# Kernel tuning notes

Hardware: AMD Instinct MI355X
Metric: run time of the kernel (lower is better)

Reference implementation:

```python
import math
import jax, jax.numpy as jnp
import numpy as np

N = 50000      # num nodes
E = 400000     # num edges
IN = 128       # in_channels
HID = 64       # hidden_channels
HEADS = 4
OUT = 32       # out_channels
TDIM = 16      # time_dim
NEG_SLOPE = 0.2
EPS = 1e-5


def setup_inputs() -> dict:
    key = jax.random.key(0)
    ks = jax.random.split(key, 20)
    s = 0.05
    # Fourier time encoder: Linear(1, TDIM) with freq-pattern weight
    freq = np.exp(np.arange(0, TDIM, 2, dtype=np.float32) * -(math.log(10000.0) / TDIM))
    tw = np.zeros((TDIM,), dtype=np.float32)
    tw[0::2] = freq
    tw[1::2] = freq
    return {
        "x": jax.random.normal(ks[0], (N, IN), jnp.float32),
        "edge_index": jax.random.randint(ks[1], (2, E), 0, N, jnp.int64),
        "edge_time": jax.random.uniform(ks[2], (E,), jnp.float32),
        "time_w": jnp.asarray(tw),
        "time_b": jax.random.normal(ks[3], (TDIM,), jnp.float32) * s,
        "proj_w": jax.random.normal(ks[4], (IN + TDIM, IN), jnp.float32) * s,
        "proj_b": jax.random.normal(ks[5], (IN,), jnp.float32) * s,
        "W1": jax.random.normal(ks[6], (IN, HEADS * HID), jnp.float32) * s,
        "a_src1": jax.random.normal(ks[7], (HEADS, HID), jnp.float32) * s,
        "a_dst1": jax.random.normal(ks[8], (HEADS, HID), jnp.float32) * s,
        "b1": jax.random.normal(ks[9], (HEADS * HID,), jnp.float32) * s,
        "g1": jnp.ones((HEADS * HID,), jnp.float32),
        "be1": jnp.zeros((HEADS * HID,), jnp.float32),
        "W2": jax.random.normal(ks[10], (HEADS * HID, OUT), jnp.float32) * s,
        "a_src2": jax.random.normal(ks[11], (1, OUT), jnp.float32) * s,
        "a_dst2": jax.random.normal(ks[12], (1, OUT), jnp.float32) * s,
        "b2": jax.random.normal(ks[13], (OUT,), jnp.float32) * s,
        "g2": jnp.ones((OUT,), jnp.float32),
        "be2": jnp.zeros((OUT,), jnp.float32),
    }


def layer_norm(h, g, b):
    mu = jnp.mean(h, axis=-1, keepdims=True)
    var = jnp.mean(jnp.square(h - mu), axis=-1, keepdims=True)
    return (h - mu) * jax.lax.rsqrt(var + EPS) * g + b


def gat_conv(x, src, dst, W, a_src, a_dst, bias, heads, ch, concat):
    """PyG GATConv (self-loops pre-appended in src/dst), inference (no dropout)."""
    n = x.shape[0]
    h = (x @ W).reshape(n, heads, ch)                       # [N,H,C]
    al_s = jnp.sum(h * a_src, axis=-1)                      # [N,H]
    al_d = jnp.sum(h * a_dst, axis=-1)                      # [N,H]
    e = al_s[src] + al_d[dst]                               # [Etot,H]
    e = jnp.where(e > 0, e, NEG_SLOPE * e)                  # leaky_relu
    m = jax.ops.segment_max(e, dst, num_segments=n)         # scatter-softmax
    ex = jnp.exp(e - m[dst])
    denom = jax.ops.segment_sum(ex, dst, num_segments=n)
    alpha = ex / denom[dst]                                 # [Etot,H]
    out = jax.ops.segment_sum(h[src] * alpha[:, :, None], dst, num_segments=n)  # [N,H,C]
    out = out.reshape(n, heads * ch) if concat else jnp.mean(out, axis=1)
    return out + bias


def reference(x, edge_index, edge_time, time_w, time_b, proj_w, proj_b,
              W1, a_src1, a_dst1, b1, g1, be1,
              W2, a_src2, a_dst2, b2, g2, be2):
    src, dst = edge_index[0], edge_index[1]
    # Fourier time encoding of edge timestamps
    tp = edge_time[:, None] * time_w + time_b               # [E,TDIM]
    even = (jnp.arange(TDIM) % 2) == 0
    t_enc = jnp.where(even, jnp.sin(tp), jnp.cos(tp))       # [E,TDIM]
    # scatter_reduce_(mean, include_self=True) onto source nodes: sum/(count+1)
    t_sum = jax.ops.segment_sum(t_enc, src, num_segments=N)
    cnt = jax.ops.segment_sum(jnp.ones((E,), x.dtype), src, num_segments=N)
    node_time = t_sum / (cnt + 1.0)[:, None]
    xin = jnp.concatenate([x, node_time], axis=-1) @ proj_w + proj_b  # [N,IN]
    # add self loops (PyG GATConv default)
    loop = jnp.arange(N, dtype=src.dtype)
    src2 = jnp.concatenate([src, loop])
    dst2 = jnp.concatenate([dst, loop])
    h = gat_conv(xin, src2, dst2, W1, a_src1, a_dst1, b1, HEADS, HID, True)
    h = jax.nn.elu(h)
    h = layer_norm(h, g1, be1)
    h = gat_conv(h, src2, dst2, W2, a_src2, a_dst2, b2, 1, OUT, False)
    h = layer_norm(h, g2, be2)
    return h
```

## Files before the change

kernel.cpp:

```cpp
#include <hip/hip_runtime.h>
#include <math.h>

#define NN 50000
#define EE 400000
#define INC 128
#define TD 16
#define H1C 256
#define OUTC 32
#define NEG 0.2f
#define PAD 64

#define EB 391
#define WB 160
#define PB 782

typedef _Float16 f16;
typedef __attribute__((ext_vector_type(8))) _Float16 f16x8;
typedef __attribute__((ext_vector_type(2))) _Float16 f16x2;
typedef __attribute__((ext_vector_type(4))) float f32x4;

__device__ __forceinline__ float leaky(float x) { return x > 0.f ? x : NEG * x; }
__device__ __forceinline__ float sel4f(const float4& v, int h) {
  return h == 0 ? v.x : h == 1 ? v.y : h == 2 ? v.z : v.w;
}

__global__ __launch_bounds__(256) void k_rank_proj(
    const int* __restrict__ ei, const float* __restrict__ et,
    int* __restrict__ deg_dst, int* __restrict__ deg_src,
    int* __restrict__ src_pad, float* __restrict__ et_pad,
    const float* __restrict__ W1, const float* __restrict__ W2,
    f16* __restrict__ W1T, f16* __restrict__ W2T,
    const float* __restrict__ x, const float* __restrict__ pw,
    const float* __restrict__ pb, f16* __restrict__ xin) {
  __shared__ f16 A[64 * 136];
  int tid = threadIdx.x;
  int b = blockIdx.x;
  if (b < EB) {
    int gid = b * 256 + tid;
    if (gid < EE / 4) {
      int4 sv = *(const int4*)(ei + gid * 4);
      int4 dv = *(const int4*)(ei + EE + gid * 4);
      float4 tv = *(const float4*)(et + gid * 4);
      int rd0 = atomicAdd(&deg_dst[dv.x], 1);
      int rd1 = atomicAdd(&deg_dst[dv.y], 1);
      int rd2 = atomicAdd(&deg_dst[dv.z], 1);
      int rd3 = atomicAdd(&deg_dst[dv.w], 1);
      int rs0 = atomicAdd(&deg_src[sv.x], 1);
      int rs1 = atomicAdd(&deg_src[sv.y], 1);
      int rs2 = atomicAdd(&deg_src[sv.z], 1);
      int rs3 = atomicAdd(&deg_src[sv.w], 1);
      if (rd0 < PAD) src_pad[dv.x * PAD + rd0] = sv.x;
      if (rd1 < PAD) src_pad[dv.y * PAD + rd1] = sv.y;
      if (rd2 < PAD) src_pad[dv.z * PAD + rd2] = sv.z;
      if (rd3 < PAD) src_pad[dv.w * PAD + rd3] = sv.w;
      if (rs0 < PAD) et_pad[sv.x * PAD + rs0] = tv.x;
      if (rs1 < PAD) et_pad[sv.y * PAD + rs1] = tv.y;
      if (rs2 < PAD) et_pad[sv.z * PAD + rs2] = tv.z;
      if (rs3 < PAD) et_pad[sv.w * PAD + rs3] = tv.w;
    }
    return;
  }
  if (b < EB + WB) {
    int idx = (b - EB) * 256 + tid;
    if (idx < 32768) {
      int c = idx >> 7, k = idx & 127;
      W1T[idx] = (f16)W1[k * 256 + c];
    } else {
      int i3 = idx - 32768;
      int c = i3 >> 8, k = i3 & 255;
      W2T[i3] = (f16)W2[k * 32 + c];
    }
    return;
  }
  int n0 = (b - EB - WB) * 64;
  int l = tid & 63, w = tid >> 6;
  for (int ci = tid; ci < 1024; ci += 256) {
    int r = ci >> 4, c8 = (ci & 15) * 8;
    int n = n0 + r;
    f16x8 hv = {};
    if (n < NN) {
      float4 v0 = *(const float4*)(x + (size_t)n * INC + c8);
      float4 v1 = *(const float4*)(x + (size_t)n * INC + c8 + 4);
      hv[0] = (f16)v0.x; hv[1] = (f16)v0.y; hv[2] = (f16)v0.z; hv[3] = (f16)v0.w;
      hv[4] = (f16)v1.x; hv[5] = (f16)v1.y; hv[6] = (f16)v1.z; hv[7] = (f16)v1.w;
    }
    *(f16x8*)(A + r * 136 + c8) = hv;
  }
  int r16 = l & 15, g = l >> 4;
  f16x8 breg[2][4];
  #pragma unroll
  for (int jj = 0; jj < 2; ++jj) {
    int col = w * 32 + jj * 16 + r16;
    #pragma unroll
    for (int kk = 0; kk < 4; ++kk)
      #pragma unroll
      for (int t = 0; t < 8; ++t)
        breg[jj][kk][t] = (f16)pw[(size_t)(kk * 32 + g * 8 + t) * 128 + col];
  }
  f32x4 acc[4][2];
  #pragma unroll
  for (int i = 0; i < 4; ++i)
    #pragma unroll
    for (int jj = 0; jj < 2; ++jj) acc[i][jj] = (f32x4){0.f, 0.f, 0.f, 0.f};
  __syncthreads();
  #pragma unroll
  for (int kk = 0; kk < 4; ++kk)
    #pragma unroll
    for (int i = 0; i < 4; ++i) {
      f16x8 a = *(const f16x8*)(A + (i * 16 + r16) * 136 + kk * 32 + g * 8);
      acc[i][0] = __builtin_amdgcn_mfma_f32_16x16x32_f16(a, breg[0][kk], acc[i][0], 0, 0, 0);
      acc[i][1] = __builtin_amdgcn_mfma_f32_16x16x32_f16(a, breg[1][kk], acc[i][1], 0, 0, 0);
    }
  #pragma unroll
  for (int i = 0; i < 4; ++i)
    #pragma unroll
    for (int jj = 0; jj < 2; ++jj) {
      int col = w * 32 + jj * 16 + r16;
      float bj = pb[col];
      #pragma unroll
      for (int q = 0; q < 4; ++q) {
        int row = n0 + i * 16 + g * 4 + q;
        if (row < NN) xin[(size_t)row * INC + col] = (f16)(acc[i][jj][q] + bj);
      }
    }
}

__global__ __launch_bounds__(256) void k_time_add(
    const int* __restrict__ deg_src, const float* __restrict__ et_pad,
    const float* __restrict__ tw, const float* __restrict__ tb,
    const float* __restrict__ pw, f16* __restrict__ xin) {
  __shared__ float nt[4][16];
  __shared__ float pwl[2048];
  int tid = threadIdx.x;
  for (int i = tid; i < 2048; i += 256) pwl[i] = pw[16384 + i];
  int lane = tid & 63, wid = tid >> 6;
  int n = blockIdx.x * 4 + wid;
  int cnt = min(deg_src[n], PAD);
  int k = lane & 15, g = lane >> 4;
  float w = tw[k], b = tb[k];
  bool isc = (k & 1);
  float v = 0.f;
  const float* ep = et_pad + (size_t)n * PAD;
  for (int i = g; i < cnt; i += 4) {
    float tp = ep[i] * w + b;
    v += isc ? __cosf(tp) : __sinf(tp);
  }
  v += __shfl_xor(v, 16);
  v += __shfl_xor(v, 32);
  if (lane < 16) nt[wid][k] = v / (float)(cnt + 1);
  __syncthreads();
  int c0 = lane * 2;
  float d0 = 0.f, d1 = 0.f;
  #pragma unroll
  for (int t = 0; t < 16; ++t) {
    float ntv = nt[wid][t];
    d0 = fmaf(ntv, pwl[t * 128 + c0], d0);
    d1 = fmaf(ntv, pwl[t * 128 + c0 + 1], d1);
  }
  f16x2* xp = (f16x2*)(xin + (size_t)n * INC + c0);
  f16x2 old = *xp;
  f16x2 nw;
  nw[0] = (f16)((float)old[0] + d0);
  nw[1] = (f16)((float)old[1] + d1);
  *xp = nw;
}

__global__ __launch_bounds__(256) void k_h1g(const f16* __restrict__ xin,
                                             const f16* __restrict__ W1T,
                                             const float* __restrict__ as1,
                                             const float* __restrict__ ad1,
                                             f16* __restrict__ h1,
                                             float* __restrict__ als,
                                             float* __restrict__ ald) {
  __shared__ f16 A[64 * 136];
  int tid = threadIdx.x, l = tid & 63, w = tid >> 6;
  int n0 = blockIdx.x * 64;
  f16x8 zero = {};
  for (int ci = tid; ci < 1024; ci += 256) {
    int r = ci >> 4, c8 = (ci & 15) * 8;
    int n = n0 + r;
    f16x8 v = (n < NN) ? *(const f16x8*)(xin + (size_t)n * INC + c8) : zero;
    *(f16x8*)(A + r * 136 + c8) = v;
  }
  int r16 = l & 15, g = l >> 4;
  f16x8 breg[4][4];
  #pragma unroll
  for (int jj = 0; jj < 4; ++jj) {
    int col = w * 64 + jj * 16 + r16;
    #pragma unroll
    for (int kk = 0; kk < 4; ++kk)
      breg[jj][kk] = *(const f16x8*)(W1T + col * 128 + kk * 32 + g * 8);
  }
  f32x4 acc[4][4];
  #pragma unroll
  for (int i = 0; i < 4; ++i)
    #pragma unroll
    for (int jj = 0; jj < 4; ++jj) acc[i][jj] = (f32x4){0.f, 0.f, 0.f, 0.f};
  __syncthreads();
  #pragma unroll
  for (int kk = 0; kk < 4; ++kk)
    #pragma unroll
    for (int i = 0; i < 4; ++i) {
      f16x8 a = *(const f16x8*)(A + (i * 16 + r16) * 136 + kk * 32 + g * 8);
      #pragma unroll
      for (int jj = 0; jj < 4; ++jj)
        acc[i][jj] = __builtin_amdgcn_mfma_f32_16x16x32_f16(a, breg[jj][kk], acc[i][jj], 0, 0, 0);
    }
  #pragma unroll
  for (int i = 0; i < 4; ++i)
    #pragma unroll
    for (int jj = 0; jj < 4; ++jj) {
      int col = w * 64 + jj * 16 + r16;
      #pragma unroll
      for (int q = 0; q < 4; ++q) {
        int row = n0 + i * 16 + g * 4 + q;
        if (row < NN) h1[(size_t)row * H1C + col] = (f16)acc[i][jj][q];
      }
    }
  float asc[4], adc[4];
  #pragma unroll
  for (int jj = 0; jj < 4; ++jj) {
    int col = w * 64 + jj * 16 + r16;
    asc[jj] = as1[col];
    adc[jj] = ad1[col];
  }
  #pragma unroll
  for (int i = 0; i < 4; ++i)
    #pragma unroll
    for (int q = 0; q < 4; ++q) {
      float ps = 0.f, pd = 0.f;
      #pragma unroll
      for (int jj = 0; jj < 4; ++jj) {
        ps = fmaf(acc[i][jj][q], asc[jj], ps);
        pd = fmaf(acc[i][jj][q], adc[jj], pd);
      }
      #pragma unroll
      for (int o = 1; o < 16; o <<= 1) {
        ps += __shfl_xor(ps, o);
        pd += __shfl_xor(pd, o);
      }
      int row = n0 + i * 16 + g * 4 + q;
      if (r16 == 0 && row < NN) {
        als[row * 4 + w] = ps;
        ald[row * 4 + w] = pd;
      }
    }
}

__global__ __launch_bounds__(256) void k_h2g(const f16* __restrict__ ln1,
                                             const f16* __restrict__ W2T,
                                             const float* __restrict__ as2,
                                             const float* __restrict__ ad2,
                                             f16* __restrict__ h2,
                                             float* __restrict__ als2,
                                             float* __restrict__ ald2) {
  __shared__ f16 A[64 * 264];
  int tid = threadIdx.x, l = tid & 63, w = tid >> 6;
  int n0 = blockIdx.x * 64;
  f16x8 zero = {};
  for (int ci = tid; ci < 2048; ci += 256) {
    int r = ci >> 5, c8 = (ci & 31) * 8;
    int n = n0 + r;
    f16x8 v = (n < NN) ? *(const f16x8*)(ln1 + (size_t)n * H1C + c8) : zero;
    *(f16x8*)(A + r * 264 + c8) = v;
  }
  int r16 = l & 15, g = l >> 4;
  f16x8 breg[2][8];
  #pragma unroll
  for (int jj = 0; jj < 2; ++jj) {
    int col = jj * 16 + r16;
    #pragma unroll
    for (int kk = 0; kk < 8; ++kk)
      breg[jj][kk] = *(const f16x8*)(W2T + col * 256 + kk * 32 + g * 8);
  }
  f32x4 acc[2];
  acc[0] = (f32x4){0.f, 0.f, 0.f, 0.f};
  acc[1] = (f32x4){0.f, 0.f, 0.f, 0.f};
  __syncthreads();
  #pragma unroll
  for (int kk = 0; kk < 8; ++kk) {
    f16x8 a = *(const f16x8*)(A + (w * 16 + r16) * 264 + kk * 32 + g * 8);
    acc[0] = __builtin_amdgcn_mfma_f32_16x16x32_f16(a, breg[0][kk], acc[0], 0, 0, 0);
    acc[1] = __builtin_amdgcn_mfma_f32_16x16x32_f16(a, breg[1][kk], acc[1], 0, 0, 0);
  }
  #pragma unroll
  for (int jj = 0; jj < 2; ++jj)
    #pragma unroll
    for (int q = 0; q < 4; ++q) {
      int row = n0 + w * 16 + g * 4 + q;
      int col = jj * 16 + r16;
      if (row < NN) h2[(size_t)row * OUTC + col] = (f16)acc[jj][q];
    }
  float as_0 = as2[r16], as_1 = as2[16 + r16];
  float ad_0 = ad2[r16], ad_1 = ad2[16 + r16];
  #pragma unroll
  for (int q = 0; q < 4; ++q) {
    float ps = acc[0][q] * as_0 + acc[1][q] * as_1;
    float pd = acc[0][q] * ad_0 + acc[1][q] * ad_1;
    #pragma unroll
    for (int o = 1; o < 16; o <<= 1) {
      ps += __shfl_xor(ps, o);
      pd += __shfl_xor(pd, o);
    }
    int row = n0 + w * 16 + g * 4 + q;
    if (r16 == 0 && row < NN) {
      als2[row] = ps;
      ald2[row] = pd;
    }
  }
}

__global__ __launch_bounds__(256) void k_agg1(
    const int* __restrict__ deg_dst, const int* __restrict__ src_pad,
    const f16* __restrict__ h1, const float* __restrict__ als,
    const float* __restrict__ ald, const float* __restrict__ b1,
    const float* __restrict__ g1, const float* __restrict__ be1,
    f16* __restrict__ ln1) {
  __shared__ int s_s[8][32];
  __shared__ float s_e[8][128];
  int tid = threadIdx.x;
  int grp = tid >> 5, l32 = tid & 31;
  int n = blockIdx.x * 8 + grp;
  int cnt = min(deg_dst[n], PAD);
  const int* sp = src_pad + (size_t)n * PAD;
  const float4 adv = *(const float4*)(ald + n * 4);
  int hh = l32 >> 3;
  int c0 = l32 * 8;
  float adh = sel4f(adv, hh);
  float seh = __expf(leaky(als[n * 4 + hh] + adh));

  f16x2 accA[4] = {}, accB[4] = {}, accC[4] = {}, accD[4] = {};
  float d = 0.f;
  for (int base = 0; base < cnt; base += 32) {
    int p = base + l32;
    if (p < cnt) {
      int sv = sp[p];
      const float4 a = *(const float4*)(als + sv * 4);
      float4 e4;
      e4.x = __expf(leaky(a.x + adv.x));
      e4.y = __expf(leaky(a.y + adv.y));
      e4.z = __expf(leaky(a.z + adv.z));
      e4.w = __expf(leaky(a.w + adv.w));
      s_s[grp][l32] = sv;
      *(float4*)(&s_e[grp][l32 * 4]) = e4;
    }
    int lim = cnt - base;
    if (lim > 32) lim = 32;
    int j = 0;
    for (; j + 4 <= lim; j += 4) {
      int sA = s_s[grp][j], sB = s_s[grp][j + 1];
      int sC = s_s[grp][j + 2], sD = s_s[grp][j + 3];
      float aA = s_e[grp][j * 4 + hh], aB = s_e[grp][(j + 1) * 4 + hh];
      float aC = s_e[grp][(j + 2) * 4 + hh], aD = s_e[grp][(j + 3) * 4 + hh];
      f16x8 hA = *(const f16x8*)(h1 + (size_t)sA * H1C + c0);
      f16x8 hB = *(const f16x8*)(h1 + (size_t)sB * H1C + c0);
      f16x8 hC = *(const f16x8*)(h1 + (size_t)sC * H1C + c0);
      f16x8 hD = *(const f16x8*)(h1 + (size_t)sD * H1C + c0);
      f16 tA = (f16)aA, tB = (f16)aB, tC = (f16)aC, tD = (f16)aD;
      f16x2 vA = {tA, tA}, vB = {tB, tB}, vC = {tC, tC}, vD = {tD, tD};
      const f16x2* pA = (const f16x2*)&hA;
      const f16x2* pB = (const f16x2*)&hB;
      const f16x2* pC = (const f16x2*)&hC;
      const f16x2* pD = (const f16x2*)&hD;
      #pragma unroll
      for (int k = 0; k < 4; ++k) {
        accA[k] = pA[k] * vA + accA[k];
        accB[k] = pB[k] * vB + accB[k];
        accC[k] = pC[k] * vC + accC[k];
        accD[k] = pD[k] * vD + accD[k];
      }
      d += (aA + aB) + (aC + aD);
    }
    for (; j + 2 <= lim; j += 2) {
      int sA = s_s[grp][j], sB = s_s[grp][j + 1];
      float aA = s_e[grp][j * 4 + hh], aB = s_e[grp][(j + 1) * 4 + hh];
      f16x8 hA = *(const f16x8*)(h1 + (size_t)sA * H1C + c0);
      f16x8 hB = *(const f16x8*)(h1 + (size_t)sB * H1C + c0);
      f16 tA = (f16)aA, tB = (f16)aB;
      f16x2 vA = {tA, tA}, vB = {tB, tB};
      const f16x2* pA = (const f16x2*)&hA;
      const f16x2* pB = (const f16x2*)&hB;
      #pragma unroll
      for (int k = 0; k < 4; ++k) {
        accA[k] = pA[k] * vA + accA[k];
        accB[k] = pB[k] * vB + accB[k];
      }
      d += aA + aB;
    }
    if (j < lim) {
      int sA = s_s[grp][j];
      float aA = s_e[grp][j * 4 + hh];
      f16x8 hA = *(const f16x8*)(h1 + (size_t)sA * H1C + c0);
      f16 tA = (f16)aA;
      f16x2 vA = {tA, tA};
      const f16x2* pA = (const f16x2*)&hA;
      #pragma unroll
      for (int k = 0; k < 4; ++k) accA[k] = pA[k] * vA + accA[k];
      d += aA;
    }
  }
  d += seh;
  float invd = __builtin_amdgcn_rcpf(d);
  f16x8 hv = *(const f16x8*)(h1 + (size_t)n * H1C + c0);
  const f16* fa = (const f16*)accA;
  const f16* fb = (const f16*)accB;
  const f16* fc = (const f16*)accC;
  const f16* fd = (const f16*)accD;
  float4 ba = *(const float4*)(b1 + c0), bb = *(const float4*)(b1 + c0 + 4);
  float v[8];
  #pragma unroll
  for (int u = 0; u < 8; ++u) {
    float bu = u < 4 ? (&ba.x)[u] : (&bb.x)[u - 4];
    float sum = ((float)fa[u] + (float)fb[u]) + ((float)fc[u] + (float)fd[u]);
    float t = fmaf((float)hv[u], seh, sum);
    t = fmaf(t, invd, bu);
    v[u] = t > 0.f ? t : (__expf(t) - 1.f);
  }
  float s1 = 0.f, s2 = 0.f;
  #pragma unroll
  for (int u = 0; u < 8; ++u) { s1 += v[u]; s2 += v[u] * v[u]; }
  #pragma unroll
  for (int o = 16; o >= 1; o >>= 1) {
    s1 += __shfl_xor(s1, o, 32);
    s2 += __shfl_xor(s2, o, 32);
  }
  float mu = s1 * (1.f / 256.f);
  float var = s2 * (1.f / 256.f) - mu * mu;
  float sc = rsqrtf(var + 1e-5f);
  float4 ga = *(const float4*)(g1 + c0), gb = *(const float4*)(g1 + c0 + 4);
  float4 ea = *(const float4*)(be1 + c0), eb = *(const float4*)(be1 + c0 + 4);
  f16x8 o8;
  #pragma unroll
  for (int u = 0; u < 8; ++u) {
    float gu = u < 4 ? (&ga.x)[u] : (&gb.x)[u - 4];
    float eu = u < 4 ? (&ea.x)[u] : (&eb.x)[u - 4];
    o8[u] = (f16)((v[u] - mu) * sc * gu + eu);
  }
  *(f16x8*)(ln1 + (size_t)n * H1C + c0) = o8;
}

__global__ __launch_bounds__(256) void k_agg2(
    const int* __restrict__ deg_dst, const int* __restrict__ src_pad,
    const f16* __restrict__ h2, const float* __restrict__ als2,
    const float* __restrict__ ald2, const float* __restrict__ b2,
    const float* __restrict__ g2, const float* __restrict__ be2,
    float* __restrict__ out) {
  int tid = threadIdx.x;
  int n = blockIdx.x * 8 + (tid >> 5);
  int ch = tid & 31;
  int cnt = min(deg_dst[n], PAD);
  const int* sp = src_pad + (size_t)n * PAD;
  float adn = ald2[n];
  float se = __expf(leaky(als2[n] + adn));
  float acc0 = (float)h2[(size_t)n * OUTC + ch] * se;
  float acc1 = 0.f, acc2 = 0.f, acc3 = 0.f;
  float d0 = se, d1 = 0.f, d2 = 0.f, d3 = 0.f;
  int i = 0;
  for (; i + 4 <= cnt; i += 4) {
    int s0 = sp[i], s1v = sp[i + 1], s2v = sp[i + 2], s3v = sp[i + 3];
    float e0 = __expf(leaky(als2[s0] + adn));
    float e1 = __expf(leaky(als2[s1v] + adn));
    float e2 = __expf(leaky(als2[s2v] + adn));
    float e3 = __expf(leaky(als2[s3v] + adn));
    acc0 = fmaf((float)h2[(size_t)s0 * OUTC + ch], e0, acc0);
    acc1 = fmaf((float)h2[(size_t)s1v * OUTC + ch], e1, acc1);
    acc2 = fmaf((float)h2[(size_t)s2v * OUTC + ch], e2, acc2);
    acc3 = fmaf((float)h2[(size_t)s3v * OUTC + ch], e3, acc3);
    d0 += e0; d1 += e1; d2 += e2; d3 += e3;
  }
  for (; i < cnt; ++i) {
    int s0 = sp[i];
    float e0 = __expf(leaky(als2[s0] + adn));
    acc0 = fmaf((float)h2[(size_t)s0 * OUTC + ch], e0, acc0);
    d0 += e0;
  }
  float invd = __builtin_amdgcn_rcpf((d0 + d1) + (d2 + d3));
  float t = fmaf((acc0 + acc1) + (acc2 + acc3), invd, b2[ch]);
  float s1 = t, s2 = t * t;
  #pragma unroll
  for (int o = 16; o >= 1; o >>= 1) {
    s1 += __shfl_xor(s1, o, 32);
    s2 += __shfl_xor(s2, o, 32);
  }
  float mu = s1 * (1.f / 32.f);
  float var = s2 * (1.f / 32.f) - mu * mu;
  float sc = rsqrtf(var + 1e-5f);
  out[(size_t)n * OUTC + ch] = (t - mu) * sc * g2[ch] + be2[ch];
}

extern "C" void kernel_launch(void* const* d_in, const int* in_sizes, int n_in,
                              void* d_out, int out_size, void* d_ws, size_t ws_size,
                              hipStream_t stream) {
  const float* x   = (const float*)d_in[0];
  const int*   ei  = (const int*)d_in[1];
  const float* et  = (const float*)d_in[2];
  const float* tw  = (const float*)d_in[3];
  const float* tb  = (const float*)d_in[4];
  const float* pw  = (const float*)d_in[5];
  const float* pb  = (const float*)d_in[6];
  const float* W1  = (const float*)d_in[7];
  const float* as1 = (const float*)d_in[8];
  const float* ad1 = (const float*)d_in[9];
  const float* b1  = (const float*)d_in[10];
  const float* g1  = (const float*)d_in[11];
  const float* be1 = (const float*)d_in[12];
  const float* W2  = (const float*)d_in[13];
  const float* as2 = (const float*)d_in[14];
  const float* ad2 = (const float*)d_in[15];
  const float* b2  = (const float*)d_in[16];
  const float* g2  = (const float*)d_in[17];
  const float* be2 = (const float*)d_in[18];

  char* ws = (char*)d_ws;
  size_t off = 0;
  auto alloc = [&](size_t bytes) {
    void* p = ws + off;
    off += (bytes + 255) & ~(size_t)255;
    return p;
  };
  f16* xin   = (f16*)alloc((size_t)NN * INC * 2);
  f16* h1    = (f16*)alloc((size_t)NN * H1C * 2);
  f16* ln1   = (f16*)alloc((size_t)NN * H1C * 2);
  f16* h2    = (f16*)alloc((size_t)NN * OUTC * 2);
  float* als1v = (float*)alloc((size_t)NN * 4 * 4);
  float* ald1v = (float*)alloc((size_t)NN * 4 * 4);
  float* als2v = (float*)alloc((size_t)NN * 4);
  float* ald2v = (float*)alloc((size_t)NN * 4);
  int*   src_pad = (int*)alloc((size_t)NN * PAD * 4);
  float* et_pad  = (float*)alloc((size_t)NN * PAD * 4);
  f16* W1T = (f16*)alloc(32768 * 2);
  f16* W2T = (f16*)alloc(8192 * 2);
  int* deg2 = (int*)alloc((size_t)NN * 2 * 4);
  int* deg_dst = deg2;
  int* deg_src = deg2 + NN;

  hipMemsetAsync(deg2, 0, (size_t)NN * 2 * 4, stream);

  const int NT64 = (NN + 63) / 64;
  k_rank_proj<<<EB + WB + PB, 256, 0, stream>>>(ei, et, deg_dst, deg_src, src_pad,
                                                et_pad, W1, W2, W1T, W2T, x, pw, pb, xin);
  k_time_add<<<NN / 4, 256, 0, stream>>>(deg_src, et_pad, tw, tb, pw, xin);
  k_h1g<<<NT64, 256, 0, stream>>>(xin, W1T, as1, ad1, h1, als1v, ald1v);
  k_agg1<<<NN / 8, 256, 0, stream>>>(deg_dst, src_pad, h1, als1v, ald1v,
                                     b1, g1, be1, ln1);
  k_h2g<<<NT64, 256, 0, stream>>>(ln1, W2T, as2, ad2, h2, als2v, ald2v);
  k_agg2<<<NN / 8, 256, 0, stream>>>(deg_dst, src_pad, h2, als2v, ald2v,
                                     b2, g2, be2, (float*)d_out);
}
```

Before: 172.4 us.

## Fuse time-encoding add into layer-1 GEMM and pad degree counters apart

Removes the separate k_time_add kernel. The Fourier time encoding, its mean, and the 16x128 projection term are now computed inside the layer-1 GEMM kernel while it stages xin into shared memory. This drops one launch and one read-modify-write pass over xin. Separately, each degree counter gets its own 128-byte slot (stride 32 ints) to cut atomic contention from false sharing. The cost is a much larger memset (about 12.8 MB instead of 0.4 MB), and the time reduction now uses only one thread per four features per node, so its loop is serial.

```diff
diff --git a/kernel.cpp b/kernel.cpp
--- a/kernel.cpp
+++ b/kernel.cpp
@@ -9,9 +9,10 @@
 #define OUTC 32
 #define NEG 0.2f
 #define PAD 64
+#define DSTRIDE 32
 
 #define EB 391
-#define WB 160
+#define WB 168
 #define PB 782
 
 typedef _Float16 f16;
@@ -29,7 +30,7 @@
     int* __restrict__ deg_dst, int* __restrict__ deg_src,
     int* __restrict__ src_pad, float* __restrict__ et_pad,
     const float* __restrict__ W1, const float* __restrict__ W2,
-    f16* __restrict__ W1T, f16* __restrict__ W2T,
+    f16* __restrict__ W1T, f16* __restrict__ W2T, f16* __restrict__ pwtT,
     const float* __restrict__ x, const float* __restrict__ pw,
     const float* __restrict__ pb, f16* __restrict__ xin) {
   __shared__ f16 A[64 * 136];
@@ -41,14 +42,14 @@
       int4 sv = *(const int4*)(ei + gid * 4);
       int4 dv = *(const int4*)(ei + EE + gid * 4);
       float4 tv = *(const float4*)(et + gid * 4);
-      int rd0 = atomicAdd(&deg_dst[dv.x], 1);
-      int rd1 = atomicAdd(&deg_dst[dv.y], 1);
-      int rd2 = atomicAdd(&deg_dst[dv.z], 1);
-      int rd3 = atomicAdd(&deg_dst[dv.w], 1);
-      int rs0 = atomicAdd(&deg_src[sv.x], 1);
-      int rs1 = atomicAdd(&deg_src[sv.y], 1);
-      int rs2 = atomicAdd(&deg_src[sv.z], 1);
-      int rs3 = atomicAdd(&deg_src[sv.w], 1);
+      int rd0 = atomicAdd(&deg_dst[dv.x * DSTRIDE], 1);
+      int rd1 = atomicAdd(&deg_dst[dv.y * DSTRIDE], 1);
+      int rd2 = atomicAdd(&deg_dst[dv.z * DSTRIDE], 1);
+      int rd3 = atomicAdd(&deg_dst[dv.w * DSTRIDE], 1);
+      int rs0 = atomicAdd(&deg_src[sv.x * DSTRIDE], 1);
+      int rs1 = atomicAdd(&deg_src[sv.y * DSTRIDE], 1);
+      int rs2 = atomicAdd(&deg_src[sv.z * DSTRIDE], 1);
+      int rs3 = atomicAdd(&deg_src[sv.w * DSTRIDE], 1);
       if (rd0 < PAD) src_pad[dv.x * PAD + rd0] = sv.x;
       if (rd1 < PAD) src_pad[dv.y * PAD + rd1] = sv.y;
       if (rd2 < PAD) src_pad[dv.z * PAD + rd2] = sv.z;
@@ -65,10 +66,13 @@
     if (idx < 32768) {
       int c = idx >> 7, k = idx & 127;
       W1T[idx] = (f16)W1[k * 256 + c];
-    } else {
+    } else if (idx < 40960) {
       int i3 = idx - 32768;
       int c = i3 >> 8, k = i3 & 255;
       W2T[i3] = (f16)W2[k * 32 + c];
+    } else if (idx < 43008) {
+      int i4 = idx - 40960;
+      pwtT[i4] = (f16)pw[16384 + i4];
     }
     return;
   }
@@ -125,62 +129,59 @@
     }
 }
 
-__global__ __launch_bounds__(256) void k_time_add(
+__global__ __launch_bounds__(256) void k_h1t(
+    const f16* __restrict__ xin, const f16* __restrict__ W1T,
+    const float* __restrict__ as1, const float* __restrict__ ad1,
     const int* __restrict__ deg_src, const float* __restrict__ et_pad,
     const float* __restrict__ tw, const float* __restrict__ tb,
-    const float* __restrict__ pw, f16* __restrict__ xin) {
-  __shared__ float nt[4][16];
-  __shared__ float pwl[2048];
-  int tid = threadIdx.x;
-  for (int i = tid; i < 2048; i += 256) pwl[i] = pw[16384 + i];
-  int lane = tid & 63, wid = tid >> 6;
-  int n = blockIdx.x * 4 + wid;
-  int cnt = min(deg_src[n], PAD);
-  int k = lane & 15, g = lane >> 4;
-  float w = tw[k], b = tb[k];
-  bool isc = (k & 1);
-  float v = 0.f;
-  const float* ep = et_pad + (size_t)n * PAD;
-  for (int i = g; i < cnt; i += 4) {
-    float tp = ep[i] * w + b;
-    v += isc ? __cosf(tp) : __sinf(tp);
-  }
-  v += __shfl_xor(v, 16);
-  v += __shfl_xor(v, 32);
-  if (lane < 16) nt[wid][k] = v / (float)(cnt + 1);
-  __syncthreads();
-  int c0 = lane * 2;
-  float d0 = 0.f, d1 = 0.f;
-  #pragma unroll
-  for (int t = 0; t < 16; ++t) {
-    float ntv = nt[wid][t];
-    d0 = fmaf(ntv, pwl[t * 128 + c0], d0);
-    d1 = fmaf(ntv, pwl[t * 128 + c0 + 1], d1);
-  }
-  f16x2* xp = (f16x2*)(xin + (size_t)n * INC + c0);
-  f16x2 old = *xp;
-  f16x2 nw;
-  nw[0] = (f16)((float)old[0] + d0);
-  nw[1] = (f16)((float)old[1] + d1);
-  *xp = nw;
-}
-
-__global__ __launch_bounds__(256) void k_h1g(const f16* __restrict__ xin,
-                                             const f16* __restrict__ W1T,
-                                             const float* __restrict__ as1,
-                                             const float* __restrict__ ad1,
-                                             f16* __restrict__ h1,
-                                             float* __restrict__ als,
-                                             float* __restrict__ ald) {
+    const f16* __restrict__ pwtT, f16* __restrict__ h1,
+    float* __restrict__ als, float* __restrict__ ald) {
   __shared__ f16 A[64 * 136];
+  __shared__ f16 pwl[16 * 128];
+  __shared__ float nt[64][16];
   int tid = threadIdx.x, l = tid & 63, w = tid >> 6;
   int n0 = blockIdx.x * 64;
+  for (int i = tid; i < 2048; i += 256)
+    pwl[i] = pwtT[i];
+  {
+    int r = tid >> 2, kq = (tid & 3) * 4;
+    int n = n0 + r;
+    int cnt = (n < NN) ? min(deg_src[n * DSTRIDE], PAD) : 0;
+    float w0 = tw[kq], w1 = tw[kq + 1], w2 = tw[kq + 2], w3 = tw[kq + 3];
+    float b0 = tb[kq], b1 = tb[kq + 1], b2 = tb[kq + 2], b3 = tb[kq + 3];
+    float v0 = 0.f, v1 = 0.f, v2 = 0.f, v3 = 0.f;
+    const float* ep = et_pad + (size_t)n * PAD;
+    for (int i = 0; i < cnt; ++i) {
+      float e = ep[i];
+      v0 += __sinf(fmaf(e, w0, b0));
+      v1 += __cosf(fmaf(e, w1, b1));
+      v2 += __sinf(fmaf(e, w2, b2));
+      v3 += __cosf(fmaf(e, w3, b3));
+    }
+    float inv = 1.f / (float)(cnt + 1);
+    nt[r][kq] = v0 * inv; nt[r][kq + 1] = v1 * inv;
+    nt[r][kq + 2] = v2 * inv; nt[r][kq + 3] = v3 * inv;
+  }
+  __syncthreads();
   f16x8 zero = {};
   for (int ci = tid; ci < 1024; ci += 256) {
     int r = ci >> 4, c8 = (ci & 15) * 8;
     int n = n0 + r;
     f16x8 v = (n < NN) ? *(const f16x8*)(xin + (size_t)n * INC + c8) : zero;
-    *(f16x8*)(A + r * 136 + c8) = v;
+    float av[8];
+    #pragma unroll
+    for (int u = 0; u < 8; ++u) av[u] = (float)v[u];
+    #pragma unroll
+    for (int t = 0; t < 16; ++t) {
+      float ntv = nt[r][t];
+      f16x8 pv = *(const f16x8*)(pwl + t * 128 + c8);
+      #pragma unroll
+      for (int u = 0; u < 8; ++u) av[u] = fmaf(ntv, (float)pv[u], av[u]);
+    }
+    f16x8 ov;
+    #pragma unroll
+    for (int u = 0; u < 8; ++u) ov[u] = (f16)av[u];
+    *(f16x8*)(A + r * 136 + c8) = ov;
   }
   int r16 = l & 15, g = l >> 4;
   f16x8 breg[4][4];
@@ -321,7 +322,7 @@
   int tid = threadIdx.x;
   int grp = tid >> 5, l32 = tid & 31;
   int n = blockIdx.x * 8 + grp;
-  int cnt = min(deg_dst[n], PAD);
+  int cnt = min(deg_dst[n * DSTRIDE], PAD);
   const int* sp = src_pad + (size_t)n * PAD;
   const float4 adv = *(const float4*)(ald + n * 4);
   int hh = l32 >> 3;
@@ -448,7 +449,7 @@
   int tid = threadIdx.x;
   int n = blockIdx.x * 8 + (tid >> 5);
   int ch = tid & 31;
-  int cnt = min(deg_dst[n], PAD);
+  int cnt = min(deg_dst[n * DSTRIDE], PAD);
   const int* sp = src_pad + (size_t)n * PAD;
   float adn = ald2[n];
   float se = __expf(leaky(als2[n] + adn));
@@ -530,17 +531,19 @@
   float* et_pad  = (float*)alloc((size_t)NN * PAD * 4);
   f16* W1T = (f16*)alloc(32768 * 2);
   f16* W2T = (f16*)alloc(8192 * 2);
-  int* deg2 = (int*)alloc((size_t)NN * 2 * 4);
-  int* deg_dst = deg2;
-  int* deg_src = deg2 + NN;
-
-  hipMemsetAsync(deg2, 0, (size_t)NN * 2 * 4, stream);
+  f16* pwtT = (f16*)alloc(2048 * 2);
+  int* deg_dst = (int*)alloc((size_t)NN * DSTRIDE * 4);
+  int* deg_src = (int*)alloc((size_t)NN * DSTRIDE * 4);
+
+  hipMemsetAsync(deg_dst, 0, (size_t)NN * DSTRIDE * 4, stream);
+  hipMemsetAsync(deg_src, 0, (size_t)NN * DSTRIDE * 4, stream);
 
   const int NT64 = (NN + 63) / 64;
   k_rank_proj<<<EB + WB + PB, 256, 0, stream>>>(ei, et, deg_dst, deg_src, src_pad,
-                                                et_pad, W1, W2, W1T, W2T, x, pw, pb, xin);
-  k_time_add<<<NN / 4, 256, 0, stream>>>(deg_src, et_pad, tw, tb, pw, xin);
-  k_h1g<<<NT64, 256, 0, stream>>>(xin, W1T, as1, ad1, h1, als1v, ald1v);
+                                                et_pad, W1, W2, W1T, W2T, pwtT,
+                                                x, pw, pb, xin);
+  k_h1t<<<NT64, 256, 0, stream>>>(xin, W1T, as1, ad1, deg_src, et_pad, tw, tb, pwtT,
+                                  h1, als1v, ald1v);
   k_agg1<<<NN / 8, 256, 0, stream>>>(deg_dst, src_pad, h1, als1v, ald1v,
                                      b1, g1, be1, ln1);
   k_h2g<<<NT64, 256, 0, stream>>>(ln1, W2T, as2, ad2, h2, als2v, ald2v);
```

After: 164.4 us. -4.6%, faster.
